# Performance work log

Measured on AMD Instinct MI355X. Metric: run time of the kernel, lower is better.

Reference implementation:

```python
import jax, jax.numpy as jnp
import numpy as np

N_NODES = 1_000_000
N_EDGES = 5_000_000


def setup_inputs() -> dict:
    key = jax.random.key(0)
    k1, k2, k3, k4 = jax.random.split(key, 4)
    x = jax.random.normal(k1, (N_NODES, 1), dtype=jnp.float32)
    edge_index = jax.random.randint(k2, (2, N_EDGES), 0, N_NODES, dtype=jnp.int64)
    # GCNConv params: lin weight (in,out) applied before propagation, bias after.
    W1 = jax.random.normal(k3, (1, 16), dtype=jnp.float32) / jnp.sqrt(1.0)
    b1 = jnp.zeros((16,), dtype=jnp.float32)
    W2 = jax.random.normal(k4, (16, 1), dtype=jnp.float32) / jnp.sqrt(16.0)
    b2 = jnp.zeros((1,), dtype=jnp.float32)
    return {"x": x, "edge_index": edge_index, "W1": W1, "b1": b1, "W2": W2, "b2": b2}


def _gcn_conv(x, W, b, src, dst, n_nodes):
    """GCNConv: out = D^{-1/2} (A + I) D^{-1/2} (x W) + b."""
    h = x @ W  # [N, F_out]
    loops = jnp.arange(n_nodes, dtype=src.dtype)
    s = jnp.concatenate([src, loops])  # [E+N]
    d = jnp.concatenate([dst, loops])
    # degree from destination index (edge weights = 1), incl. self loops
    deg = jax.ops.segment_sum(jnp.ones_like(d, dtype=h.dtype), d, num_segments=n_nodes)
    dinv = jnp.where(deg > 0, jax.lax.rsqrt(deg), 0.0)
    norm = dinv[s] * dinv[d]  # [E+N]
    msg = h[s] * norm[:, None]  # gather + scale, [E+N, F_out]
    out = jax.ops.segment_sum(msg, d, num_segments=n_nodes)  # scatter-add
    return out + b


def reference(x, edge_index, W1, b1, W2, b2):
    src, dst = edge_index[0], edge_index[1]
    n = x.shape[0]
    h = jax.nn.relu(_gcn_conv(x, W1, b1, src, dst, n))
    return _gcn_conv(h, W2, b2, src, dst, n)
```

## Files before the change

kernel.cpp:

```cpp
#include <hip/hip_runtime.h>

#define THREADS 256
#define BSH 11
#define BSZ 2048
#define NBMAX 512
#define ST 8192
#define SCT 512
#define EPT 16
#define BT 1024
#define SMASK 0xFFFFFu


__global__ void k_init(unsigned* __restrict__ gcur, unsigned C, int NB) {
    int t = threadIdx.x;
    if (t < NB) gcur[t] = (unsigned)t * C;
}

__global__ void __launch_bounds__(SCT)
k_scatter(const int* __restrict__ src,
          const int* __restrict__ dst, int E,
          unsigned* __restrict__ gcur,
          unsigned* __restrict__ packed, unsigned C, int NB) {
    __shared__ unsigned tcnt[NBMAX];
    __shared__ unsigned gb[NBMAX];

    int tid = threadIdx.x;
    int lo = blockIdx.x * ST;
    int cnt = E - lo; if (cnt > ST) cnt = ST;

    tcnt[tid] = 0u;
    __syncthreads();

    unsigned jreg[EPT], rreg[EPT], rank[EPT];
    #pragma unroll
    for (int kk = 0; kk < EPT / 4; ++kk) {
        int g = kk * SCT + tid;
        int base = g * 4;
        if (base + 3 < cnt) {
            int4 d4 = *(const int4*)(dst + lo + base);
            int4 s4 = *(const int4*)(src + lo + base);
            unsigned j0 = (unsigned)d4.x >> BSH;
            unsigned j1 = (unsigned)d4.y >> BSH;
            unsigned j2 = (unsigned)d4.z >> BSH;
            unsigned j3 = (unsigned)d4.w >> BSH;
            jreg[kk*4+0] = j0; rreg[kk*4+0] = (unsigned)s4.x | (((unsigned)d4.x & (BSZ-1)) << 20);
            jreg[kk*4+1] = j1; rreg[kk*4+1] = (unsigned)s4.y | (((unsigned)d4.y & (BSZ-1)) << 20);
            jreg[kk*4+2] = j2; rreg[kk*4+2] = (unsigned)s4.z | (((unsigned)d4.z & (BSZ-1)) << 20);
            jreg[kk*4+3] = j3; rreg[kk*4+3] = (unsigned)s4.w | (((unsigned)d4.w & (BSZ-1)) << 20);
            rank[kk*4+0] = atomicAdd(&tcnt[j0], 1u);
            rank[kk*4+1] = atomicAdd(&tcnt[j1], 1u);
            rank[kk*4+2] = atomicAdd(&tcnt[j2], 1u);
            rank[kk*4+3] = atomicAdd(&tcnt[j3], 1u);
        } else {
            #pragma unroll
            for (int c = 0; c < 4; ++c) {
                int idx = base + c;
                if (idx < cnt) {
                    int d = dst[lo + idx];
                    unsigned jj = (unsigned)d >> BSH;
                    jreg[kk*4+c] = jj;
                    rreg[kk*4+c] = (unsigned)src[lo + idx] | (((unsigned)d & (BSZ-1)) << 20);
                    rank[kk*4+c] = atomicAdd(&tcnt[jj], 1u);
                } else {
                    jreg[kk*4+c] = ~0u;
                }
            }
        }
    }
    __syncthreads();

    {
        unsigned v = tcnt[tid];
        if (v) gb[tid] = atomicAdd(&gcur[tid], v);
    }
    __syncthreads();

    #pragma unroll
    for (int k = 0; k < EPT; ++k) {
        unsigned jj = jreg[k];
        if (jj != ~0u) {
            unsigned pos = gb[jj] + rank[k];
            if (pos < (jj + 1u) * C) packed[pos] = rreg[k];
        }
    }
}

__global__ void k_deg(const unsigned* __restrict__ packed,
                      const unsigned* __restrict__ gcur, unsigned C,
                      const float* __restrict__ x,
                      float* __restrict__ dinv, float* __restrict__ y, int N) {
    int j = blockIdx.x;
    __shared__ unsigned cntl[BSZ];
    for (int t = threadIdx.x; t < BSZ; t += BT) cntl[t] = 0u;
    __syncthreads();
    unsigned e0 = (unsigned)j * C;
    unsigned e1 = gcur[j]; if (e1 > e0 + C) e1 = e0 + C;
    unsigned tid = threadIdx.x;
    unsigned nv4 = (e1 - e0) >> 2;
    unsigned g = tid;
    for (; g + BT < nv4; g += 2u * BT) {
        uint4 a = *(const uint4*)(packed + e0 + (size_t)g * 4u);
        uint4 b = *(const uint4*)(packed + e0 + (size_t)(g + BT) * 4u);
        atomicAdd(&cntl[a.x >> 20], 1u);
        atomicAdd(&cntl[a.y >> 20], 1u);
        atomicAdd(&cntl[a.z >> 20], 1u);
        atomicAdd(&cntl[a.w >> 20], 1u);
        atomicAdd(&cntl[b.x >> 20], 1u);
        atomicAdd(&cntl[b.y >> 20], 1u);
        atomicAdd(&cntl[b.z >> 20], 1u);
        atomicAdd(&cntl[b.w >> 20], 1u);
    }
    for (; g < nv4; g += BT) {
        uint4 a = *(const uint4*)(packed + e0 + (size_t)g * 4u);
        atomicAdd(&cntl[a.x >> 20], 1u);
        atomicAdd(&cntl[a.y >> 20], 1u);
        atomicAdd(&cntl[a.z >> 20], 1u);
        atomicAdd(&cntl[a.w >> 20], 1u);
    }
    for (unsigned e = e0 + nv4 * 4u + tid; e < e1; e += BT)
        atomicAdd(&cntl[packed[e] >> 20], 1u);
    __syncthreads();
    int base = j << BSH;
    for (int t = threadIdx.x; t < BSZ; t += BT) {
        int v = base + t;
        if (v < N) {
            float d = rsqrtf((float)cntl[t] + 1.0f);
            dinv[v] = d;
            y[v] = x[v] * d;
        }
    }
}

__global__ void k_acc1(const unsigned* __restrict__ packed,
                       const unsigned* __restrict__ gcur, unsigned C,
                       const float* __restrict__ y,
                       const float* __restrict__ dinv,
                       const float* __restrict__ W1,
                       const float* __restrict__ b1,
                       const float* __restrict__ W2,
                       float* __restrict__ zy, int N, int F) {
    int j = blockIdx.x;
    __shared__ float acc[BSZ];
    __shared__ float w1s[64], b1s[64], w2s[64];
    for (int t = threadIdx.x; t < BSZ; t += BT) acc[t] = 0.f;
    if (threadIdx.x < (unsigned)F) {
        w1s[threadIdx.x] = W1[threadIdx.x];
        b1s[threadIdx.x] = b1[threadIdx.x];
        w2s[threadIdx.x] = W2[threadIdx.x];
    }
    __syncthreads();
    unsigned e0 = (unsigned)j * C;
    unsigned e1 = gcur[j]; if (e1 > e0 + C) e1 = e0 + C;
    unsigned tid = threadIdx.x;
    unsigned nv4 = (e1 - e0) >> 2;
    unsigned g = tid;
    for (; g + BT < nv4; g += 2u * BT) {
        uint4 a = *(const uint4*)(packed + e0 + (size_t)g * 4u);
        uint4 b = *(const uint4*)(packed + e0 + (size_t)(g + BT) * 4u);
        float v0 = y[a.x & SMASK], v1 = y[a.y & SMASK];
        float v2 = y[a.z & SMASK], v3 = y[a.w & SMASK];
        float v4 = y[b.x & SMASK], v5 = y[b.y & SMASK];
        float v6 = y[b.z & SMASK], v7 = y[b.w & SMASK];
        atomicAdd(&acc[a.x >> 20], v0);
        atomicAdd(&acc[a.y >> 20], v1);
        atomicAdd(&acc[a.z >> 20], v2);
        atomicAdd(&acc[a.w >> 20], v3);
        atomicAdd(&acc[b.x >> 20], v4);
        atomicAdd(&acc[b.y >> 20], v5);
        atomicAdd(&acc[b.z >> 20], v6);
        atomicAdd(&acc[b.w >> 20], v7);
    }
    for (; g < nv4; g += BT) {
        uint4 a = *(const uint4*)(packed + e0 + (size_t)g * 4u);
        float v0 = y[a.x & SMASK], v1 = y[a.y & SMASK];
        float v2 = y[a.z & SMASK], v3 = y[a.w & SMASK];
        atomicAdd(&acc[a.x >> 20], v0);
        atomicAdd(&acc[a.y >> 20], v1);
        atomicAdd(&acc[a.z >> 20], v2);
        atomicAdd(&acc[a.w >> 20], v3);
    }
    for (unsigned e = e0 + nv4 * 4u + tid; e < e1; e += BT) {
        unsigned p = packed[e];
        atomicAdd(&acc[p >> 20], y[p & SMASK]);
    }
    __syncthreads();
    int base = j << BSH;
    for (int t = threadIdx.x; t < BSZ; t += BT) {
        int v = base + t;
        if (v < N) {
            float d = dinv[v];
            float agg = d * (acc[t] + y[v]);
            float z = 0.f;
            for (int f = 0; f < F; ++f) {
                float h = fmaf(w1s[f], agg, b1s[f]);
                h = fmaxf(h, 0.f);
                z = fmaf(h, w2s[f], z);
            }
            zy[v] = z * d;
        }
    }
}

__global__ void k_out(const unsigned* __restrict__ packed,
                      const unsigned* __restrict__ gcur, unsigned C,
                      const float* __restrict__ zy,
                      const float* __restrict__ dinv,
                      const float* __restrict__ b2,
                      float* __restrict__ out, int N) {
    int j = blockIdx.x;
    __shared__ float acc[BSZ];
    for (int t = threadIdx.x; t < BSZ; t += BT) acc[t] = 0.f;
    __syncthreads();
    unsigned e0 = (unsigned)j * C;
    unsigned e1 = gcur[j]; if (e1 > e0 + C) e1 = e0 + C;
    unsigned tid = threadIdx.x;
    unsigned nv4 = (e1 - e0) >> 2;
    unsigned g = tid;
    for (; g + BT < nv4; g += 2u * BT) {
        uint4 a = *(const uint4*)(packed + e0 + (size_t)g * 4u);
        uint4 b = *(const uint4*)(packed + e0 + (size_t)(g + BT) * 4u);
        float v0 = zy[a.x & SMASK], v1 = zy[a.y & SMASK];
        float v2 = zy[a.z & SMASK], v3 = zy[a.w & SMASK];
        float v4 = zy[b.x & SMASK], v5 = zy[b.y & SMASK];
        float v6 = zy[b.z & SMASK], v7 = zy[b.w & SMASK];
        atomicAdd(&acc[a.x >> 20], v0);
        atomicAdd(&acc[a.y >> 20], v1);
        atomicAdd(&acc[a.z >> 20], v2);
        atomicAdd(&acc[a.w >> 20], v3);
        atomicAdd(&acc[b.x >> 20], v4);
        atomicAdd(&acc[b.y >> 20], v5);
        atomicAdd(&acc[b.z >> 20], v6);
        atomicAdd(&acc[b.w >> 20], v7);
    }
    for (; g < nv4; g += BT) {
        uint4 a = *(const uint4*)(packed + e0 + (size_t)g * 4u);
        float v0 = zy[a.x & SMASK], v1 = zy[a.y & SMASK];
        float v2 = zy[a.z & SMASK], v3 = zy[a.w & SMASK];
        atomicAdd(&acc[a.x >> 20], v0);
        atomicAdd(&acc[a.y >> 20], v1);
        atomicAdd(&acc[a.z >> 20], v2);
        atomicAdd(&acc[a.w >> 20], v3);
    }
    for (unsigned e = e0 + nv4 * 4u + tid; e < e1; e += BT) {
        unsigned p = packed[e];
        atomicAdd(&acc[p >> 20], zy[p & SMASK]);
    }
    __syncthreads();
    int base = j << BSH;
    for (int t = threadIdx.x; t < BSZ; t += BT) {
        int v = base + t;
        if (v < N)
            out[v] = fmaf(dinv[v], acc[t] + zy[v], b2[0]);
    }
}


__global__ void f_zero3(float* __restrict__ a, float* __restrict__ b,
                        float* __restrict__ c, int N) {
    int i = blockIdx.x * blockDim.x + threadIdx.x;
    int stride = gridDim.x * blockDim.x;
    for (int v = i; v < N; v += stride) { a[v] = 0.f; b[v] = 0.f; c[v] = 0.f; }
}
__global__ void f_deg(const int* __restrict__ dst, int E, float* __restrict__ degf) {
    int i = blockIdx.x * blockDim.x + threadIdx.x;
    int stride = gridDim.x * blockDim.x;
    for (int e = i; e < E; e += stride) atomicAdd(&degf[dst[e]], 1.0f);
}
__global__ void f_dinv(float* __restrict__ d, int N) {
    int v = blockIdx.x * blockDim.x + threadIdx.x;
    if (v < N) d[v] = rsqrtf(d[v] + 1.0f);
}
__global__ void f_edge1(const int* __restrict__ src, const int* __restrict__ dst,
                        const float* __restrict__ x, const float* __restrict__ dinv,
                        float* __restrict__ acc1, int E) {
    int i = blockIdx.x * blockDim.x + threadIdx.x;
    int stride = gridDim.x * blockDim.x;
    for (int e = i; e < E; e += stride) {
        int s = src[e];
        atomicAdd(&acc1[dst[e]], x[s] * dinv[s]);
    }
}
__global__ void f_node2(const float* __restrict__ dinv, const float* __restrict__ acc1,
                        const float* __restrict__ x, const float* __restrict__ W1,
                        const float* __restrict__ b1, const float* __restrict__ W2,
                        float* __restrict__ zy, int N, int F) {
    int v = blockIdx.x * blockDim.x + threadIdx.x;
    if (v < N) {
        float d = dinv[v];
        float agg = d * (acc1[v] + x[v] * d);
        float z = 0.f;
        for (int f = 0; f < F; ++f) {
            float h = fmaf(W1[f], agg, b1[f]);
            h = h > 0.f ? h : 0.f;
            z = fmaf(h, W2[f], z);
        }
        zy[v] = z * d;
    }
}
__global__ void f_edge2(const int* __restrict__ src, const int* __restrict__ dst,
                        const float* __restrict__ zy, float* __restrict__ out, int E) {
    int i = blockIdx.x * blockDim.x + threadIdx.x;
    int stride = gridDim.x * blockDim.x;
    for (int e = i; e < E; e += stride) atomicAdd(&out[dst[e]], zy[src[e]]);
}
__global__ void f_node3(const float* __restrict__ dinv, const float* __restrict__ zy,
                        const float* __restrict__ b2, float* __restrict__ out, int N) {
    int v = blockIdx.x * blockDim.x + threadIdx.x;
    if (v < N) out[v] = fmaf(dinv[v], out[v] + zy[v], b2[0]);
}


extern "C" void kernel_launch(void* const* d_in, const int* in_sizes, int n_in,
                              void* d_out, int out_size, void* d_ws, size_t ws_size,
                              hipStream_t stream) {
    const float* x  = (const float*)d_in[0];
    const int*   ei = (const int*)d_in[1];
    const float* W1 = (const float*)d_in[2];
    const float* b1 = (const float*)d_in[3];
    const float* W2 = (const float*)d_in[4];
    const float* b2 = (const float*)d_in[5];
    float* out = (float*)d_out;

    const int N = in_sizes[0];
    const int E = in_sizes[1] / 2;
    const int F = in_sizes[2];

    const int* src = ei;
    const int* dst = ei + E;

    const int NB = (N + BSZ - 1) >> BSH;

    unsigned mean = (unsigned)(E / (NB > 0 ? NB : 1));
    unsigned C = (mean + mean / 8u + 1024u + 3u) & ~3u;

    size_t off_packed = 0;
    size_t off_gc     = (off_packed + (size_t)NB * C * 4 + 15) & ~(size_t)15;
    size_t off_dinv   = (off_gc + (size_t)NBMAX * 4 + 15) & ~(size_t)15;
    size_t off_y      = off_dinv + (size_t)N * 4;
    size_t off_zy     = off_y + (size_t)N * 4;
    size_t need       = off_zy + (size_t)N * 4;

    bool ok = (ws_size >= need) && (NB >= 1) && (NB <= NBMAX) &&
              (N <= (1 << 20)) && (F <= 64) && (E > 0);

    char* ws = (char*)d_ws;
    if (ok) {
        unsigned* packed = (unsigned*)(ws + off_packed);
        unsigned* gcur   = (unsigned*)(ws + off_gc);
        float*    dinv   = (float*)(ws + off_dinv);
        float*    y      = (float*)(ws + off_y);
        float*    zy     = (float*)(ws + off_zy);

        int scatBlocks = (E + ST - 1) / ST;

        k_init   <<<1, NBMAX, 0, stream>>>(gcur, C, NB);
        k_scatter<<<scatBlocks, SCT, 0, stream>>>(src, dst, E, gcur, packed, C, NB);
        k_deg    <<<NB, BT, 0, stream>>>(packed, gcur, C, x, dinv, y, N);
        k_acc1   <<<NB, BT, 0, stream>>>(packed, gcur, C, y, dinv, W1, b1, W2, zy, N, F);
        k_out    <<<NB, BT, 0, stream>>>(packed, gcur, C, zy, dinv, b2, out, N);
    } else {
        float* dinv = (float*)(ws);
        float* acc1 = (float*)(ws + (size_t)N * 4);
        float* zy   = (float*)(ws + (size_t)N * 8);
        int nodeBlocks = (N + THREADS - 1) / THREADS;
        int edgeBlocks = (E + THREADS - 1) / THREADS;
        if (edgeBlocks > 2048) edgeBlocks = 2048;
        f_zero3<<<2048, THREADS, 0, stream>>>(dinv, acc1, out, N);
        f_deg  <<<edgeBlocks, THREADS, 0, stream>>>(dst, E, dinv);
        f_dinv <<<nodeBlocks, THREADS, 0, stream>>>(dinv, N);
        f_edge1<<<edgeBlocks, THREADS, 0, stream>>>(src, dst, x, dinv, acc1, E);
        f_node2<<<nodeBlocks, THREADS, 0, stream>>>(dinv, acc1, x, W1, b1, W2, zy, N, F);
        f_edge2<<<edgeBlocks, THREADS, 0, stream>>>(src, dst, zy, out, E);
        f_node3<<<nodeBlocks, THREADS, 0, stream>>>(dinv, zy, b2, out, N);
    }
}
```

Baseline: 123.1 us.

## Stage scatter output in LDS sorted by bucket for coalesced writes; nontemporal loads

The scatter kernel now computes a block-wide exclusive prefix scan of the per-bucket counts. It places each edge into a shared-memory staging array sorted by bucket, then writes the array out in contiguous runs so global stores coalesce instead of landing at scattered positions. Edge-index loads and packed-array reads in the later kernels use nontemporal loads to reduce cache pollution. The cost is about 48KB of extra LDS per block, which may lower occupancy, plus an added scan and sync stage.

Result: no change. 122.7 us (-0.4%).

```diff
diff --git a/kernel.cpp b/kernel.cpp
--- a/kernel.cpp
+++ b/kernel.cpp
@@ -10,6 +10,9 @@
 #define BT 1024
 #define SMASK 0xFFFFFu
 
+typedef unsigned u32x4_t __attribute__((ext_vector_type(4)));
+typedef int      i32x4_t __attribute__((ext_vector_type(4)));
+
 
 __global__ void k_init(unsigned* __restrict__ gcur, unsigned C, int NB) {
     int t = threadIdx.x;
@@ -22,7 +25,11 @@
           unsigned* __restrict__ gcur,
           unsigned* __restrict__ packed, unsigned C, int NB) {
     __shared__ unsigned tcnt[NBMAX];
+    __shared__ unsigned toff[NBMAX];
     __shared__ unsigned gb[NBMAX];
+    __shared__ unsigned wsum[8];
+    __shared__ unsigned sorted[ST];
+    __shared__ unsigned short jarr[ST];
 
     int tid = threadIdx.x;
     int lo = blockIdx.x * ST;
@@ -37,8 +44,8 @@
         int g = kk * SCT + tid;
         int base = g * 4;
         if (base + 3 < cnt) {
-            int4 d4 = *(const int4*)(dst + lo + base);
-            int4 s4 = *(const int4*)(src + lo + base);
+            i32x4_t d4 = __builtin_nontemporal_load((const i32x4_t*)(dst + lo + base));
+            i32x4_t s4 = __builtin_nontemporal_load((const i32x4_t*)(src + lo + base));
             unsigned j0 = (unsigned)d4.x >> BSH;
             unsigned j1 = (unsigned)d4.y >> BSH;
             unsigned j2 = (unsigned)d4.z >> BSH;
@@ -71,6 +78,28 @@
 
     {
         unsigned v = tcnt[tid];
+        unsigned incl = v;
+        #pragma unroll
+        for (int off = 1; off < 64; off <<= 1) {
+            unsigned u = __shfl_up(incl, off, 64);
+            if ((tid & 63) >= off) incl += u;
+        }
+        unsigned wid = tid >> 6;
+        if ((tid & 63) == 63) wsum[wid] = incl;
+        __syncthreads();
+        if (tid < 8) {
+            unsigned wi = wsum[tid];
+            #pragma unroll
+            for (int off = 1; off < 8; off <<= 1) {
+                unsigned u = __shfl_up(wi, off, 8);
+                if (tid >= off) wi += u;
+            }
+            wsum[tid] = wi;
+        }
+        __syncthreads();
+        unsigned wbase = wid ? wsum[wid - 1] : 0u;
+        unsigned excl = wbase + incl - v;
+        toff[tid] = excl;
         if (v) gb[tid] = atomicAdd(&gcur[tid], v);
     }
     __syncthreads();
@@ -79,9 +108,18 @@
     for (int k = 0; k < EPT; ++k) {
         unsigned jj = jreg[k];
         if (jj != ~0u) {
-            unsigned pos = gb[jj] + rank[k];
-            if (pos < (jj + 1u) * C) packed[pos] = rreg[k];
-        }
+            unsigned p = toff[jj] + rank[k];
+            sorted[p] = rreg[k];
+            jarr[p] = (unsigned short)jj;
+        }
+    }
+    __syncthreads();
+
+    for (int p = tid; p < cnt; p += SCT) {
+        unsigned jj = jarr[p];
+        unsigned pos = gb[jj] + ((unsigned)p - toff[jj]);
+        if (pos < (jj + 1u) * C)
+            __builtin_nontemporal_store(sorted[p], &packed[pos]);
     }
 }
 
@@ -99,8 +137,8 @@
     unsigned nv4 = (e1 - e0) >> 2;
     unsigned g = tid;
     for (; g + BT < nv4; g += 2u * BT) {
-        uint4 a = *(const uint4*)(packed + e0 + (size_t)g * 4u);
-        uint4 b = *(const uint4*)(packed + e0 + (size_t)(g + BT) * 4u);
+        u32x4_t a = __builtin_nontemporal_load((const u32x4_t*)(packed + e0 + (size_t)g * 4u));
+        u32x4_t b = __builtin_nontemporal_load((const u32x4_t*)(packed + e0 + (size_t)(g + BT) * 4u));
         atomicAdd(&cntl[a.x >> 20], 1u);
         atomicAdd(&cntl[a.y >> 20], 1u);
         atomicAdd(&cntl[a.z >> 20], 1u);
@@ -111,7 +149,7 @@
         atomicAdd(&cntl[b.w >> 20], 1u);
     }
     for (; g < nv4; g += BT) {
-        uint4 a = *(const uint4*)(packed + e0 + (size_t)g * 4u);
+        u32x4_t a = __builtin_nontemporal_load((const u32x4_t*)(packed + e0 + (size_t)g * 4u));
         atomicAdd(&cntl[a.x >> 20], 1u);
         atomicAdd(&cntl[a.y >> 20], 1u);
         atomicAdd(&cntl[a.z >> 20], 1u);
@@ -155,8 +193,8 @@
     unsigned nv4 = (e1 - e0) >> 2;
     unsigned g = tid;
     for (; g + BT < nv4; g += 2u * BT) {
-        uint4 a = *(const uint4*)(packed + e0 + (size_t)g * 4u);
-        uint4 b = *(const uint4*)(packed + e0 + (size_t)(g + BT) * 4u);
+        u32x4_t a = __builtin_nontemporal_load((const u32x4_t*)(packed + e0 + (size_t)g * 4u));
+        u32x4_t b = __builtin_nontemporal_load((const u32x4_t*)(packed + e0 + (size_t)(g + BT) * 4u));
         float v0 = y[a.x & SMASK], v1 = y[a.y & SMASK];
         float v2 = y[a.z & SMASK], v3 = y[a.w & SMASK];
         float v4 = y[b.x & SMASK], v5 = y[b.y & SMASK];
@@ -171,7 +209,7 @@
         atomicAdd(&acc[b.w >> 20], v7);
     }
     for (; g < nv4; g += BT) {
-        uint4 a = *(const uint4*)(packed + e0 + (size_t)g * 4u);
+        u32x4_t a = __builtin_nontemporal_load((const u32x4_t*)(packed + e0 + (size_t)g * 4u));
         float v0 = y[a.x & SMASK], v1 = y[a.y & SMASK];
         float v2 = y[a.z & SMASK], v3 = y[a.w & SMASK];
         atomicAdd(&acc[a.x >> 20], v0);
@@ -217,8 +255,8 @@
     unsigned nv4 = (e1 - e0) >> 2;
     unsigned g = tid;
     for (; g + BT < nv4; g += 2u * BT) {
-        uint4 a = *(const uint4*)(packed + e0 + (size_t)g * 4u);
-        uint4 b = *(const uint4*)(packed + e0 + (size_t)(g + BT) * 4u);
+        u32x4_t a = __builtin_nontemporal_load((const u32x4_t*)(packed + e0 + (size_t)g * 4u));
+        u32x4_t b = __builtin_nontemporal_load((const u32x4_t*)(packed + e0 + (size_t)(g + BT) * 4u));
         float v0 = zy[a.x & SMASK], v1 = zy[a.y & SMASK];
         float v2 = zy[a.z & SMASK], v3 = zy[a.w & SMASK];
         float v4 = zy[b.x & SMASK], v5 = zy[b.y & SMASK];
@@ -233,7 +271,7 @@
         atomicAdd(&acc[b.w >> 20], v7);
     }
     for (; g < nv4; g += BT) {
-        uint4 a = *(const uint4*)(packed + e0 + (size_t)g * 4u);
+        u32x4_t a = __builtin_nontemporal_load((const u32x4_t*)(packed + e0 + (size_t)g * 4u));
         float v0 = zy[a.x & SMASK], v1 = zy[a.y & SMASK];
         float v2 = zy[a.z & SMASK], v3 = zy[a.w & SMASK];
         atomicAdd(&acc[a.x >> 20], v0);
```

## Stage scatter through LDS bucket-sorted buffer and use nontemporal packed loads

Applied to the files above, without the earlier changes.

The scatter kernel now prefix-scans per-bucket counts in shared memory, writes edges into a locally bucket-sorted LDS buffer, and then writes them to global memory in contiguous runs per bucket, replacing the random per-thread stores. The goal is more coalesced global writes during the binning pass. The aggregation kernels also switch the streaming reads of packed edges to nontemporal loads to reduce cache pollution. This adds about 50KB of LDS and a serial scan with many barriers, which can lower occupancy of the scatter kernel.

New measurement: 111.0 us. 1.11x faster.

```diff
diff --git a/kernel.cpp b/kernel.cpp
--- a/kernel.cpp
+++ b/kernel.cpp
@@ -10,6 +10,8 @@
 #define BT 1024
 #define SMASK 0xFFFFFu
 
+typedef unsigned u32x4_t __attribute__((ext_vector_type(4)));
+
 
 __global__ void k_init(unsigned* __restrict__ gcur, unsigned C, int NB) {
     int t = threadIdx.x;
@@ -22,7 +24,11 @@
           unsigned* __restrict__ gcur,
           unsigned* __restrict__ packed, unsigned C, int NB) {
     __shared__ unsigned tcnt[NBMAX];
+    __shared__ unsigned toff[NBMAX];
     __shared__ unsigned gb[NBMAX];
+    __shared__ unsigned sh[NBMAX];
+    __shared__ unsigned sorted[ST];
+    __shared__ unsigned short jarr[ST];
 
     int tid = threadIdx.x;
     int lo = blockIdx.x * ST;
@@ -69,8 +75,18 @@
     }
     __syncthreads();
 
+    unsigned v = tcnt[tid];
+    sh[tid] = v;
+    __syncthreads();
+    for (int off = 1; off < NBMAX; off <<= 1) {
+        unsigned t = (tid >= off) ? sh[tid - off] : 0u;
+        __syncthreads();
+        sh[tid] += t;
+        __syncthreads();
+    }
     {
-        unsigned v = tcnt[tid];
+        unsigned excl = sh[tid] - v;
+        toff[tid] = excl;
         if (v) gb[tid] = atomicAdd(&gcur[tid], v);
     }
     __syncthreads();
@@ -79,9 +95,17 @@
     for (int k = 0; k < EPT; ++k) {
         unsigned jj = jreg[k];
         if (jj != ~0u) {
-            unsigned pos = gb[jj] + rank[k];
-            if (pos < (jj + 1u) * C) packed[pos] = rreg[k];
+            unsigned p = toff[jj] + rank[k];
+            sorted[p] = rreg[k];
+            jarr[p] = (unsigned short)jj;
         }
+    }
+    __syncthreads();
+
+    for (int p = tid; p < cnt; p += SCT) {
+        unsigned jj = jarr[p];
+        unsigned pos = gb[jj] + ((unsigned)p - toff[jj]);
+        if (pos < (jj + 1u) * C) packed[pos] = sorted[p];
     }
 }
 
@@ -155,8 +179,8 @@
     unsigned nv4 = (e1 - e0) >> 2;
     unsigned g = tid;
     for (; g + BT < nv4; g += 2u * BT) {
-        uint4 a = *(const uint4*)(packed + e0 + (size_t)g * 4u);
-        uint4 b = *(const uint4*)(packed + e0 + (size_t)(g + BT) * 4u);
+        u32x4_t a = __builtin_nontemporal_load((const u32x4_t*)(packed + e0 + (size_t)g * 4u));
+        u32x4_t b = __builtin_nontemporal_load((const u32x4_t*)(packed + e0 + (size_t)(g + BT) * 4u));
         float v0 = y[a.x & SMASK], v1 = y[a.y & SMASK];
         float v2 = y[a.z & SMASK], v3 = y[a.w & SMASK];
         float v4 = y[b.x & SMASK], v5 = y[b.y & SMASK];
@@ -171,7 +195,7 @@
         atomicAdd(&acc[b.w >> 20], v7);
     }
     for (; g < nv4; g += BT) {
-        uint4 a = *(const uint4*)(packed + e0 + (size_t)g * 4u);
+        u32x4_t a = __builtin_nontemporal_load((const u32x4_t*)(packed + e0 + (size_t)g * 4u));
         float v0 = y[a.x & SMASK], v1 = y[a.y & SMASK];
         float v2 = y[a.z & SMASK], v3 = y[a.w & SMASK];
         atomicAdd(&acc[a.x >> 20], v0);
@@ -217,8 +241,8 @@
     unsigned nv4 = (e1 - e0) >> 2;
     unsigned g = tid;
     for (; g + BT < nv4; g += 2u * BT) {
-        uint4 a = *(const uint4*)(packed + e0 + (size_t)g * 4u);
-        uint4 b = *(const uint4*)(packed + e0 + (size_t)(g + BT) * 4u);
+        u32x4_t a = __builtin_nontemporal_load((const u32x4_t*)(packed + e0 + (size_t)g * 4u));
+        u32x4_t b = __builtin_nontemporal_load((const u32x4_t*)(packed + e0 + (size_t)(g + BT) * 4u));
         float v0 = zy[a.x & SMASK], v1 = zy[a.y & SMASK];
         float v2 = zy[a.z & SMASK], v3 = zy[a.w & SMASK];
         float v4 = zy[b.x & SMASK], v5 = zy[b.y & SMASK];
@@ -233,7 +257,7 @@
         atomicAdd(&acc[b.w >> 20], v7);
     }
     for (; g < nv4; g += BT) {
-        uint4 a = *(const uint4*)(packed + e0 + (size_t)g * 4u);
+        u32x4_t a = __builtin_nontemporal_load((const u32x4_t*)(packed + e0 + (size_t)g * 4u));
         float v0 = zy[a.x & SMASK], v1 = zy[a.y & SMASK];
         float v2 = zy[a.z & SMASK], v3 = zy[a.w & SMASK];
         atomicAdd(&acc[a.x >> 20], v0);
```
